# Kernel optimization log

Measured on AMD Instinct MI355X. Metric: run time of the kernel, lower is better.

Reference implementation:

```python
import jax, jax.numpy as jnp
import numpy as np

B, L, D, H = 2, 2048, 1024, 16
DK = D // H


def setup_inputs() -> dict:
    key = jax.random.key(0)
    ks = jax.random.split(key, 12)
    s = 1.0 / np.sqrt(D)
    inp = {
        "query": jax.random.normal(ks[0], (B, L, D), jnp.float32),
        "key_": jax.random.normal(ks[1], (B, L, D), jnp.float32),
        "value": jax.random.normal(ks[2], (B, L, D), jnp.float32),
        # causal boolean mask, broadcast over heads: (B, 1, L_q, L_k)
        "mask": jnp.broadcast_to(jnp.tril(jnp.ones((L, L), jnp.bool_)), (B, 1, L, L)),
        "w_q": jax.random.uniform(ks[3], (D, D), jnp.float32, -s, s),
        "b_q": jax.random.uniform(ks[4], (D,), jnp.float32, -s, s),
        "w_k": jax.random.uniform(ks[5], (D, D), jnp.float32, -s, s),
        "b_k": jax.random.uniform(ks[6], (D,), jnp.float32, -s, s),
        "w_v": jax.random.uniform(ks[7], (D, D), jnp.float32, -s, s),
        "b_v": jax.random.uniform(ks[8], (D,), jnp.float32, -s, s),
        "w_o": jax.random.uniform(ks[9], (D, D), jnp.float32, -s, s),
        "b_o": jax.random.uniform(ks[10], (D,), jnp.float32, -s, s),
    }
    return inp


def reference(query, key_, value, mask, w_q, b_q, w_k, b_k, w_v, b_v, w_o, b_o):
    # torch nn.Linear: y = x @ W.T + b, weight shape (out, in)
    Q = query @ w_q.T + b_q
    K = key_ @ w_k.T + b_k
    V = value @ w_v.T + b_v
    # (B, L, H, DK) -> (B, H, L, DK)
    Q = Q.reshape(B, L, H, DK).transpose(0, 2, 1, 3)
    K = K.reshape(B, L, H, DK).transpose(0, 2, 1, 3)
    V = V.reshape(B, L, H, DK).transpose(0, 2, 1, 3)
    scaling = jnp.sqrt(jnp.float32(DK))
    scores = jnp.einsum("bhqd,bhkd->bhqk", Q, K) / scaling  # (B,H,L,L)
    scores = jnp.where(mask, scores, jnp.float32(-1e9))
    attn = jax.nn.softmax(scores, axis=-1)
    out = jnp.einsum("bhqk,bhkd->bhqd", attn, V)  # (B,H,L,DK)
    out = out.transpose(0, 2, 1, 3).reshape(B, L, D)
    return out @ w_o.T + b_o
```

## Files before the change

### kernel.cpp

```cpp
#include <hip/hip_runtime.h>
#include <stdint.h>

#define Bb 2
#define Ll 2048
#define Dd 1024
#define Hh 16
#define DKd 64
#define Mm (Bb*Ll)

typedef __bf16 bf16_t;
typedef __bf16 bf16x8 __attribute__((ext_vector_type(8)));
typedef float f32x4 __attribute__((ext_vector_type(4)));
typedef unsigned u32x2 __attribute__((ext_vector_type(2)));

#define AS1C(p) ((const __attribute__((address_space(1))) void*)(p))
#define AS3(p)  ((__attribute__((address_space(3))) void*)(p))

__device__ __forceinline__ unsigned short bfu(float f){
  return __builtin_bit_cast(unsigned short, (bf16_t)f);
}
__device__ __forceinline__ void wait_vm4(){ asm volatile("s_waitcnt vmcnt(4)" ::: "memory"); }
__device__ __forceinline__ void wait_vm6(){ asm volatile("s_waitcnt vmcnt(6)" ::: "memory"); }
__device__ __forceinline__ void wait_vm0(){ asm volatile("s_waitcnt vmcnt(0)" ::: "memory"); }
__device__ __forceinline__ void wait_lgkm0(){ asm volatile("s_waitcnt lgkmcnt(0)" ::: "memory"); }
__device__ __forceinline__ void bar(){
  __builtin_amdgcn_sched_barrier(0);
  __builtin_amdgcn_s_barrier();
  __builtin_amdgcn_sched_barrier(0);
}

struct Cvt4 { const float* in[4]; ushort4* out[4]; };

__global__ void cvt_multi(Cvt4 a, int n4){
  const int z = blockIdx.y;
  int i = blockIdx.x*256 + threadIdx.x;
  if (i < n4){
    float4 v = ((const float4*)a.in[z])[i];
    ushort4 o; o.x=bfu(v.x); o.y=bfu(v.y); o.z=bfu(v.z); o.w=bfu(v.w);
    a.out[z][i] = o;
  }
}

struct GemmArgs {
  const void*   A[3];
  const bf16_t* W[3];
  const float*  bias[3];
  void*         out[3];
  float         scale[3];
  int           mode[3];
};

#define BKs 64

__global__ __launch_bounds__(256) void gemm128_ra(GemmArgs ga, int M, int N, int K)
{
  const int z = blockIdx.z;
  const float*  __restrict__ A  = (const float*)ga.A[z];
  const bf16_t* __restrict__ Bw = ga.W[z];
  const float*  __restrict__ bias = ga.bias[z];
  void* __restrict__ out = ga.out[z];
  const float scale = ga.scale[z];
  const int mode = ga.mode[z];

  __shared__ bf16_t As[128*BKs];
  __shared__ bf16_t Bs[2][128*BKs];
  const int tid = threadIdx.x;
  const int lane = tid & 63;
  const int w = tid >> 6;
  const int m0 = blockIdx.x * 128;
  const int n0 = blockIdx.y * 128;
  const int wr = (w >> 1) * 64, wc = (w & 1) * 64;
  const int lrow16 = lane & 15;
  const int kgrp = lane >> 4;

  const int brow8 = lane >> 3;
  const int bcb   = (lane & 7) * 16;
  const int arow  = tid >> 3;
  const int awb   = ((tid & 7) * 16) ^ ((arow & 7) << 4);

  f32x4 ar[4][2];

  auto loadA = [&](int k0){
#pragma unroll
    for (int i = 0; i < 4; ++i) {
      const float* p = A + (size_t)(m0 + i*32 + arow)*K + k0 + (tid & 7)*8;
      ar[i][0] = *(const f32x4*)p;
      ar[i][1] = *(const f32x4*)(p + 4);
    }
  };
  auto writeA = [&](){
#pragma unroll
    for (int i = 0; i < 4; ++i) {
      bf16x8 a;
      a[0]=(bf16_t)ar[i][0][0]; a[1]=(bf16_t)ar[i][0][1];
      a[2]=(bf16_t)ar[i][0][2]; a[3]=(bf16_t)ar[i][0][3];
      a[4]=(bf16_t)ar[i][1][0]; a[5]=(bf16_t)ar[i][1][1];
      a[6]=(bf16_t)ar[i][1][2]; a[7]=(bf16_t)ar[i][1][3];
      *(bf16x8*)((char*)As + (i*32 + arow)*128 + awb) = a;
    }
  };
  auto stageB = [&](int k0, int buf){
#pragma unroll
    for (int i = 0; i < 4; ++i) {
      int c = i*4 + w;
      int row = c*8 + brow8;
      int sb = bcb ^ ((row & 7) << 4);
      __builtin_amdgcn_global_load_lds(AS1C((const char*)(Bw + (size_t)(n0+row)*K + k0) + sb),
                                       AS3((char*)&Bs[buf][0] + c*1024), 16, 0, 0);
    }
  };

  f32x4 acc[4][4] = {};

  loadA(0);
  stageB(0, 0);
  wait_vm0();
  writeA();
  wait_lgkm0();
  bar();

  const int KT = K / BKs;
  int cur = 0;
  for (int kt = 0; kt < KT; ++kt) {
    const bool pre = (kt + 1 < KT);
    if (pre) {
      loadA((kt+1)*BKs);
      stageB((kt+1)*BKs, cur^1);
    }
#pragma unroll
    for (int ks = 0; ks < 2; ++ks) {
      const int kbyte = ks*64 + kgrp*16;
      bf16x8 af[4], bfr[4];
#pragma unroll
      for (int m = 0; m < 4; m++) {
        int row = wr + m*16 + lrow16;
        af[m] = *(const bf16x8*)((const char*)As + row*128 + (kbyte ^ ((row & 7) << 4)));
      }
#pragma unroll
      for (int n = 0; n < 4; n++) {
        int row = wc + n*16 + lrow16;
        bfr[n] = *(const bf16x8*)((const char*)&Bs[cur][0] + row*128 + (kbyte ^ ((row & 7) << 4)));
      }
#pragma unroll
      for (int m = 0; m < 4; m++)
#pragma unroll
        for (int n = 0; n < 4; n++)
          acc[m][n] = __builtin_amdgcn_mfma_f32_16x16x32_bf16(af[m], bfr[n], acc[m][n], 0, 0, 0);
    }
    if (pre) wait_vm4();
    bar();
    if (pre) {
      writeA();
      wait_vm0();
      wait_lgkm0();
    }
    bar();
    cur ^= 1;
  }

#pragma unroll
  for (int m = 0; m < 4; m++)
#pragma unroll
    for (int n = 0; n < 4; n++) {
      const int row0 = m0 + wr + m*16 + kgrp*4;
      const int col  = n0 + wc + n*16 + lrow16;
      const float bcol = bias[col];
      if (mode == 2) {
        int b = row0 >> 11, l0 = row0 & 2047;
        int h = col >> 6, dk = col & 63;
        ushort4 u;
        u.x = bfu((acc[m][n][0] + bcol) * scale);
        u.y = bfu((acc[m][n][1] + bcol) * scale);
        u.z = bfu((acc[m][n][2] + bcol) * scale);
        u.w = bfu((acc[m][n][3] + bcol) * scale);
        *(ushort4*)((unsigned short*)out + ((size_t)((b<<4) + h)*DKd + dk)*Ll + l0) = u;
      } else {
#pragma unroll
        for (int i = 0; i < 4; i++) {
          int row = row0 + i;
          float v = (acc[m][n][i] + bcol) * scale;
          if (mode == 1) {
            ((float*)out)[(size_t)row*N + col] = v;
          } else {
            int b = row >> 11, l = row & 2047;
            int h = col >> 6, dk = col & 63;
            ((unsigned short*)out)[((size_t)((b<<4) + h)*Ll + l)*DKd + dk] = bfu(v);
          }
        }
      }
    }
}

#define BM 128
#define BN 64

__device__ __forceinline__ void stage_tile(
    const bf16_t* __restrict__ A, const bf16_t* __restrict__ Bw,
    int m0, int n0, int K, int k0, bf16_t* As, bf16_t* Bs,
    int w, int srow, int scol)
{
#pragma unroll
  for (int i = 0; i < 4; i++) {
    int c = i*4 + w;
    int row = c*8 + srow;
    int sc = scol ^ ((row & 7) << 3);
    __builtin_amdgcn_global_load_lds(AS1C(A + (size_t)(m0+row)*K + k0 + sc),
                                     AS3(As + c*512), 16, 0, 0);
  }
#pragma unroll
  for (int i = 0; i < 2; i++) {
    int c = i*4 + w;
    int row = c*8 + srow;
    int sc = scol ^ ((row & 7) << 3);
    __builtin_amdgcn_global_load_lds(AS1C(Bw + (size_t)(n0+row)*K + k0 + sc),
                                     AS3(Bs + c*512), 16, 0, 0);
  }
}

__global__ __launch_bounds__(256) void gemm_bt(GemmArgs ga, int M, int N, int K)
{
  const int z = blockIdx.z;
  const bf16_t* __restrict__ A  = (const bf16_t*)ga.A[z];
  const bf16_t* __restrict__ Bw = ga.W[z];
  const float*  __restrict__ bias = ga.bias[z];
  void* __restrict__ out = ga.out[z];
  const float scale = ga.scale[z];
  const int mode = ga.mode[z];

  __shared__ bf16_t As[2][BM*BKs];
  __shared__ bf16_t Bs[2][BN*BKs];
  const int tid = threadIdx.x;
  const int lane = tid & 63;
  const int w = tid >> 6;
  const int m0 = blockIdx.x * BM;
  const int n0 = blockIdx.y * BN;
  const int wr = (w >> 1) * 64, wc = (w & 1) * 32;
  const int lrow16 = lane & 15;
  const int kgrp = lane >> 4;
  const int srow = lane >> 3;
  const int scol = (lane & 7) * 8;

  f32x4 acc[4][2] = {};

  stage_tile(A, Bw, m0, n0, K, 0, As[0], Bs[0], w, srow, scol);

  const int KT = K / BKs;
  int cur = 0;
  for (int kt = 0; kt < KT; ++kt) {
    if (kt + 1 < KT) {
      stage_tile(A, Bw, m0, n0, K, (kt+1)*BKs, As[cur^1], Bs[cur^1], w, srow, scol);
      wait_vm6();
    } else {
      wait_vm0();
    }
    bar();
#pragma unroll
    for (int ks = 0; ks < 2; ++ks) {
      const int kbyte = ks*64 + kgrp*16;
      bf16x8 af[4], bfr[2];
#pragma unroll
      for (int m = 0; m < 4; m++) {
        int row = wr + m*16 + lrow16;
        af[m] = *(const bf16x8*)((const char*)As[cur] + row*128 + (kbyte ^ ((row & 7) << 4)));
      }
#pragma unroll
      for (int n = 0; n < 2; n++) {
        int row = wc + n*16 + lrow16;
        bfr[n] = *(const bf16x8*)((const char*)Bs[cur] + row*128 + (kbyte ^ ((row & 7) << 4)));
      }
#pragma unroll
      for (int m = 0; m < 4; m++)
#pragma unroll
        for (int n = 0; n < 2; n++)
          acc[m][n] = __builtin_amdgcn_mfma_f32_16x16x32_bf16(af[m], bfr[n], acc[m][n], 0, 0, 0);
    }
    bar();
    cur ^= 1;
  }

#pragma unroll
  for (int m = 0; m < 4; m++)
#pragma unroll
    for (int n = 0; n < 2; n++) {
      const int row0 = m0 + wr + m*16 + kgrp*4;
      const int col  = n0 + wc + n*16 + lrow16;
      const float bcol = bias[col];
      if (mode == 2) {
        int b = row0 >> 11, l0 = row0 & 2047;
        int h = col >> 6, dk = col & 63;
        ushort4 u;
        u.x = bfu((acc[m][n][0] + bcol) * scale);
        u.y = bfu((acc[m][n][1] + bcol) * scale);
        u.z = bfu((acc[m][n][2] + bcol) * scale);
        u.w = bfu((acc[m][n][3] + bcol) * scale);
        *(ushort4*)((unsigned short*)out + ((size_t)((b<<4) + h)*DKd + dk)*Ll + l0) = u;
      } else {
#pragma unroll
        for (int i = 0; i < 4; i++) {
          int row = row0 + i;
          float v = (acc[m][n][i] + bcol) * scale;
          if (mode == 1) {
            ((float*)out)[(size_t)row*N + col] = v;
          } else {
            int b = row >> 11, l = row & 2047;
            int h = col >> 6, dk = col & 63;
            ((unsigned short*)out)[((size_t)((b<<4) + h)*Ll + l)*DKd + dk] = bfu(v);
          }
        }
      }
    }
}

#define KVB 64

__global__ __launch_bounds__(256) void attn_kernel(
    const bf16_t* __restrict__ Qh, const bf16_t* __restrict__ Kh,
    const bf16_t* __restrict__ VTg, unsigned short* __restrict__ Oa)
{
  const int id = blockIdx.x;
  const int x = id & 7;
  const int rest = id >> 3;
  const int hq = rest >> 4;
  const int j  = rest & 15;
  const int bh = x + 8*hq;
  const int sA = j;
  const int qtB = 31 - j;

  const int tid = threadIdx.x, lane = tid & 63, w = tid >> 6;
  const int r = lane & 15, g = lane >> 4;

  const bf16_t* Qp  = Qh  + (size_t)bh * Ll * DKd;
  const bf16_t* Kp  = Kh  + (size_t)bh * Ll * DKd;
  const bf16_t* VTp = VTg + (size_t)bh * Ll * DKd;

  __shared__ bf16_t Klds[2][64*64];
  __shared__ bf16_t Vlds[2][64*64];
  __shared__ bf16_t Plds[4][16*64];

  int q0 = j * 64;
  bf16x8 qf[2], qB[2];
#pragma unroll
  for (int ks = 0; ks < 2; ++ks) {
    qf[ks] = *(const bf16x8*)(Qp + (size_t)(q0 + w*16 + r)*DKd + ks*32 + g*8);
    qB[ks] = *(const bf16x8*)(Qp + (size_t)(qtB*64 + w*16 + r)*DKd + ks*32 + g*8);
  }

  bf16x8 ones;
#pragma unroll
  for (int jj = 0; jj < 8; ++jj) ones[jj] = (bf16_t)1.0f;

  f32x4 accO[4] = {};
  f32x4 accL = {};
  float mrow = -1e30f;

  const int krow_l = lane >> 3;
  const int kcol_l = ((lane & 7)*16) ^ (krow_l << 4);
  char* Pw = (char*)&Plds[w][0];
  const int rsw = (r & 7) << 4;
  const int b_ = bh >> 4, h_ = bh & 15;

  auto pre_tiles = [&](int kv, int buf){
#pragma unroll
    for (int i = 0; i < 2; ++i) {
      int c = i*4 + w;
      __builtin_amdgcn_global_load_lds(
        AS1C((const char*)Kp + (size_t)(kv*KVB + c*8 + krow_l)*128 + kcol_l),
        AS3((char*)&Klds[buf][0] + c*1024), 16, 0, 0);
      __builtin_amdgcn_global_load_lds(
        AS1C((const char*)VTp + (size_t)(c*8 + krow_l)*4096 + kv*128 + kcol_l),
        AS3((char*)&Vlds[buf][0] + c*1024), 16, 0, 0);
    }
  };

  pre_tiles(0, 0);

  int cur = 0;
  for (int s = 0; s < 33; ++s) {
    if (s < 32) {
      int kv2 = (s < sA) ? s + 1 : s - sA;
      pre_tiles(kv2, cur^1);
      wait_vm4();
    } else {
      wait_vm0();
    }
    bar();

    const int kv0 = ((s <= sA) ? s : s - sA - 1) * KVB;

    const char* Kbase = (const char*)&Klds[cur][0];
    f32x4 sv[4] = {};
    __builtin_amdgcn_s_setprio(1);
#pragma unroll
    for (int ks = 0; ks < 2; ++ks) {
      const int kbyte = ks*64 + g*16;
#pragma unroll
      for (int n = 0; n < 4; ++n) {
        int row = n*16 + r;
        bf16x8 kf = *(const bf16x8*)(Kbase + row*128 + (kbyte ^ ((row & 7) << 4)));
        sv[n] = __builtin_amdgcn_mfma_f32_16x16x32_bf16(kf, qf[ks], sv[n], 0, 0, 0);
      }
    }
    __builtin_amdgcn_s_setprio(0);

    if (s == sA || s == 32) {
      const int qg = q0 + w*16 + r;
#pragma unroll
      for (int n = 0; n < 4; ++n)
#pragma unroll
        for (int i = 0; i < 4; ++i)
          if (kv0 + n*16 + g*4 + i > qg) sv[n][i] = -1e30f;
    }

    float m0 = fmaxf(fmaxf(sv[0][0], sv[0][1]), sv[0][2]);
    float m1 = fmaxf(fmaxf(sv[0][3], sv[1][0]), sv[1][1]);
    float m2 = fmaxf(fmaxf(sv[1][2], sv[1][3]), sv[2][0]);
    float m3 = fmaxf(fmaxf(sv[2][1], sv[2][2]), sv[2][3]);
    float m4 = fmaxf(fmaxf(sv[3][0], sv[3][1]), sv[3][2]);
    float mx = fmaxf(fmaxf(fmaxf(m0, m1), m2), fmaxf(fmaxf(m3, m4), sv[3][3]));
    if (__any(mx > mrow + 8.f)) {
      mx = fmaxf(mx, __shfl_xor(mx, 16));
      mx = fmaxf(mx, __shfl_xor(mx, 32));
      float mnew = fmaxf(mrow, mx);
      float corr = __builtin_amdgcn_exp2f(mrow - mnew);
      float c0 = __shfl(corr, g*4 + 0);
      float c1 = __shfl(corr, g*4 + 1);
      float c2 = __shfl(corr, g*4 + 2);
      float c3 = __shfl(corr, g*4 + 3);
#pragma unroll
      for (int n = 0; n < 4; ++n) {
        accO[n][0] *= c0; accO[n][1] *= c1; accO[n][2] *= c2; accO[n][3] *= c3;
      }
      accL[0] *= c0; accL[1] *= c1; accL[2] *= c2; accL[3] *= c3;
      mrow = mnew;
    }
#pragma unroll
    for (int n = 0; n < 4; ++n)
#pragma unroll
      for (int i = 0; i < 4; ++i)
        sv[n][i] = __builtin_amdgcn_exp2f(sv[n][i] - mrow);

#pragma unroll
    for (int n = 0; n < 4; ++n) {
      unsigned lo = (unsigned)bfu(sv[n][0]) | ((unsigned)bfu(sv[n][1]) << 16);
      unsigned hi = (unsigned)bfu(sv[n][2]) | ((unsigned)bfu(sv[n][3]) << 16);
      u32x2 pk; pk[0] = lo; pk[1] = hi;
      *(u32x2*)(Pw + r*128 + ((n*32 + g*8) ^ rsw)) = pk;
    }

    const char* Vbase = (const char*)&Vlds[cur][0];
    __builtin_amdgcn_s_setprio(1);
#pragma unroll
    for (int ks = 0; ks < 2; ++ks) {
      const int kbyte = ks*64 + g*16;
      bf16x8 pa = *(const bf16x8*)(Pw + r*128 + (kbyte ^ rsw));
      accL = __builtin_amdgcn_mfma_f32_16x16x32_bf16(pa, ones, accL, 0, 0, 0);
#pragma unroll
      for (int n = 0; n < 4; ++n) {
        int row = n*16 + r;
        bf16x8 vf = *(const bf16x8*)(Vbase + row*128 + (kbyte ^ ((row & 7) << 4)));
        accO[n] = __builtin_amdgcn_mfma_f32_16x16x32_bf16(pa, vf, accO[n], 0, 0, 0);
      }
    }
    __builtin_amdgcn_s_setprio(0);

    if (s == sA) {
#pragma unroll
      for (int i = 0; i < 4; ++i) {
        float inv = 1.f / accL[i];
        int q = q0 + w*16 + g*4 + i;
#pragma unroll
        for (int n = 0; n < 4; ++n)
          Oa[((size_t)(b_*Ll + q))*Dd + h_*DKd + n*16 + r] = bfu(accO[n][i] * inv);
      }
      q0 = qtB * 64;
      qf[0] = qB[0]; qf[1] = qB[1];
#pragma unroll
      for (int n = 0; n < 4; ++n) accO[n] = f32x4{};
      accL = f32x4{};
      mrow = -1e30f;
    }

    bar();
    cur ^= 1;
  }

#pragma unroll
  for (int i = 0; i < 4; ++i) {
    float inv = 1.f / accL[i];
    int q = q0 + w*16 + g*4 + i;
#pragma unroll
    for (int n = 0; n < 4; ++n)
      Oa[((size_t)(b_*Ll + q))*Dd + h_*DKd + n*16 + r] = bfu(accO[n][i] * inv);
  }
}

extern "C" void kernel_launch(void* const* d_in, const int* in_sizes, int n_in,
                              void* d_out, int out_size, void* d_ws, size_t ws_size,
                              hipStream_t stream)
{
  const float* q  = (const float*)d_in[0];
  const float* k  = (const float*)d_in[1];
  const float* v  = (const float*)d_in[2];
  const float* wq = (const float*)d_in[4];
  const float* bq = (const float*)d_in[5];
  const float* wk = (const float*)d_in[6];
  const float* bk = (const float*)d_in[7];
  const float* wv = (const float*)d_in[8];
  const float* bv = (const float*)d_in[9];
  const float* wo = (const float*)d_in[10];
  const float* bo = (const float*)d_in[11];

  char* ws = (char*)d_ws;
  bf16_t* Wq = (bf16_t*)(ws + 25165824);
  bf16_t* Wk = (bf16_t*)(ws + 27262976);
  bf16_t* Wv = (bf16_t*)(ws + 29360128);
  bf16_t* Wo = (bf16_t*)(ws + 31457280);
  bf16_t* Qh = (bf16_t*)(ws + 33554432);
  bf16_t* Kh = (bf16_t*)(ws + 41943040);
  bf16_t* VT = (bf16_t*)(ws + 50331648);
  bf16_t* Oa = (bf16_t*)(ws + 58720256);

  const int NW4 = Dd * Dd / 4;

  Cvt4 cv;
  cv.in[0]=wq; cv.out[0]=(ushort4*)Wq;
  cv.in[1]=wk; cv.out[1]=(ushort4*)Wk;
  cv.in[2]=wv; cv.out[2]=(ushort4*)Wv;
  cv.in[3]=wo; cv.out[3]=(ushort4*)Wo;
  cvt_multi<<<dim3(NW4/256, 4), 256, 0, stream>>>(cv, NW4);

  const float qscale = 0.125f * 1.4426950408889634f;
  GemmArgs gqkv;
  gqkv.A[0]=q; gqkv.A[1]=k; gqkv.A[2]=v;
  gqkv.W[0]=Wq; gqkv.W[1]=Wk; gqkv.W[2]=Wv;
  gqkv.bias[0]=bq; gqkv.bias[1]=bk; gqkv.bias[2]=bv;
  gqkv.out[0]=Qh; gqkv.out[1]=Kh; gqkv.out[2]=VT;
  gqkv.scale[0]=qscale; gqkv.scale[1]=1.0f; gqkv.scale[2]=1.0f;
  gqkv.mode[0]=0; gqkv.mode[1]=0; gqkv.mode[2]=2;
  gemm128_ra<<<dim3(Mm/128, Dd/128, 3), 256, 0, stream>>>(gqkv, Mm, Dd, Dd);

  attn_kernel<<<dim3(512), 256, 0, stream>>>(Qh, Kh, VT, (unsigned short*)Oa);

  GemmArgs go;
  go.A[0]=Oa; go.A[1]=Oa; go.A[2]=Oa;
  go.W[0]=Wo; go.W[1]=Wo; go.W[2]=Wo;
  go.bias[0]=bo; go.bias[1]=bo; go.bias[2]=bo;
  go.out[0]=d_out; go.out[1]=d_out; go.out[2]=d_out;
  go.scale[0]=1.0f; go.scale[1]=1.0f; go.scale[2]=1.0f;
  go.mode[0]=1; go.mode[1]=1; go.mode[2]=1;
  gemm_bt<<<dim3(Mm/BM, Dd/BN, 1), 256, 0, stream>>>(go, Mm, Dd, Dd);
}
```

Before: 107.8 us.

## Prefetch A tiles two stages ahead with double register buffers in projection GEMM

The projection GEMM now keeps two register buffers for the fp32 A tile and issues the global load for tile k+2 while tile k is being computed, with explicit vmcnt waits (8/12) sized to the outstanding loads. The K loop is unrolled by two with a hardcoded trip count of 16 tiles, plus a peeled epilogue. This is meant to hide global-load latency for A behind more MFMA work. It costs more VGPRs, which may lower occupancy, and it assumes K == 16*BKs.

```diff
diff --git a/kernel.cpp b/kernel.cpp
--- a/kernel.cpp
+++ b/kernel.cpp
@@ -19,9 +19,11 @@
 __device__ __forceinline__ unsigned short bfu(float f){
   return __builtin_bit_cast(unsigned short, (bf16_t)f);
 }
-__device__ __forceinline__ void wait_vm4(){ asm volatile("s_waitcnt vmcnt(4)" ::: "memory"); }
-__device__ __forceinline__ void wait_vm6(){ asm volatile("s_waitcnt vmcnt(6)" ::: "memory"); }
-__device__ __forceinline__ void wait_vm0(){ asm volatile("s_waitcnt vmcnt(0)" ::: "memory"); }
+__device__ __forceinline__ void wait_vm0(){  asm volatile("s_waitcnt vmcnt(0)"  ::: "memory"); }
+__device__ __forceinline__ void wait_vm4(){  asm volatile("s_waitcnt vmcnt(4)"  ::: "memory"); }
+__device__ __forceinline__ void wait_vm6(){  asm volatile("s_waitcnt vmcnt(6)"  ::: "memory"); }
+__device__ __forceinline__ void wait_vm8(){  asm volatile("s_waitcnt vmcnt(8)"  ::: "memory"); }
+__device__ __forceinline__ void wait_vm12(){ asm volatile("s_waitcnt vmcnt(12)" ::: "memory"); }
 __device__ __forceinline__ void wait_lgkm0(){ asm volatile("s_waitcnt lgkmcnt(0)" ::: "memory"); }
 __device__ __forceinline__ void bar(){
   __builtin_amdgcn_sched_barrier(0);
@@ -78,9 +80,9 @@
   const int arow  = tid >> 3;
   const int awb   = ((tid & 7) * 16) ^ ((arow & 7) << 4);
 
-  f32x4 ar[4][2];
-
-  auto loadA = [&](int k0){
+  f32x4 arA[4][2], arB[4][2];
+
+  auto loadA_into = [&](int k0, f32x4 (&ar)[4][2]){
 #pragma unroll
     for (int i = 0; i < 4; ++i) {
       const float* p = A + (size_t)(m0 + i*32 + arow)*K + k0 + (tid & 7)*8;
@@ -88,7 +90,7 @@
       ar[i][1] = *(const f32x4*)(p + 4);
     }
   };
-  auto writeA = [&](){
+  auto writeA_from = [&](f32x4 (&ar)[4][2]){
 #pragma unroll
     for (int i = 0; i < 4; ++i) {
       bf16x8 a;
@@ -111,22 +113,9 @@
   };
 
   f32x4 acc[4][4] = {};
-
-  loadA(0);
-  stageB(0, 0);
-  wait_vm0();
-  writeA();
-  wait_lgkm0();
-  bar();
-
-  const int KT = K / BKs;
   int cur = 0;
-  for (int kt = 0; kt < KT; ++kt) {
-    const bool pre = (kt + 1 < KT);
-    if (pre) {
-      loadA((kt+1)*BKs);
-      stageB((kt+1)*BKs, cur^1);
-    }
+
+  auto compute = [&](){
 #pragma unroll
     for (int ks = 0; ks < 2; ++ks) {
       const int kbyte = ks*64 + kgrp*16;
@@ -147,16 +136,51 @@
         for (int n = 0; n < 4; n++)
           acc[m][n] = __builtin_amdgcn_mfma_f32_16x16x32_bf16(af[m], bfr[n], acc[m][n], 0, 0, 0);
     }
-    if (pre) wait_vm4();
+  };
+
+  loadA_into(0, arA);
+  __builtin_amdgcn_sched_barrier(0);
+  stageB(0, 0);
+  __builtin_amdgcn_sched_barrier(0);
+  loadA_into(BKs, arB);
+  __builtin_amdgcn_sched_barrier(0);
+  wait_vm8();
+  writeA_from(arA);
+  wait_lgkm0();
+  bar();
+
+  auto step = [&](int kt, f32x4 (&arNext)[4][2], f32x4 (&arTgt)[4][2]){
+    stageB((kt+1)*BKs, cur^1);
+    __builtin_amdgcn_sched_barrier(0);
+    loadA_into((kt+2)*BKs, arTgt);
+    __builtin_amdgcn_sched_barrier(0);
+    compute();
+    wait_vm12();
     bar();
-    if (pre) {
-      writeA();
-      wait_vm0();
-      wait_lgkm0();
-    }
+    writeA_from(arNext);
+    wait_vm8();
+    wait_lgkm0();
     bar();
     cur ^= 1;
-  }
+  };
+
+  for (int kt = 0; kt < 14; kt += 2) {
+    step(kt,   arB, arA);
+    step(kt+1, arA, arB);
+  }
+
+  stageB(15*BKs, cur^1);
+  __builtin_amdgcn_sched_barrier(0);
+  compute();
+  wait_vm4();
+  bar();
+  writeA_from(arB);
+  wait_vm0();
+  wait_lgkm0();
+  bar();
+  cur ^= 1;
+
+  compute();
 
 #pragma unroll
   for (int m = 0; m < 4; m++)
```

New measurement: 117.2 us, median of 4. 1.09x slower.
